# Kernel optimization log

Measured on AMD Instinct MI355X. Metric: run time of the kernel, lower is better.

Reference implementation:

```python
import jax, jax.numpy as jnp
import numpy as np

B, L, D = 4, 1024, 768
HH = 12            # BERT attention heads
E, M = 30, 60      # entities / mentions per sample
P = E * (E - 1)    # 870 head-tail entity pairs
R = 97             # relation classes
BLK = 64           # block_size
NH = D // BLK      # 12 EGAT heads / bilinear groups
MIN = 1e-10


def setup_inputs():
    key = jax.random.key(0)
    ks = jax.random.split(key, 16)
    context = jax.random.normal(ks[0], (B, L, D), jnp.float32) * 0.1
    attention = jax.random.uniform(ks[1], (B, HH, L, L), jnp.float32)
    attention = attention / attention.sum(-1, keepdims=True)  # row-stochastic like softmax attn
    pos = jax.random.randint(ks[2], (B, M), 0, L)
    mention_map = (jnp.arange(L)[None, None, :] == pos[..., None]).astype(jnp.float32)  # [B,M,L] one-hot
    entity_map = (jnp.arange(M)[None, :] // 2 == jnp.arange(E)[:, None]).astype(jnp.float32)
    entity_map = jnp.broadcast_to(entity_map[None], (B, E, M))  # entity e owns mentions 2e,2e+1
    pairs = np.array([(i, j) for i in range(E) for j in range(E) if i != j], np.int64)
    hts = jnp.broadcast_to(jnp.asarray(pairs)[None], (B, P, 2))
    w = lambda k, s: jax.random.normal(k, s, jnp.float32) * 0.02
    return dict(
        context=context, attention=attention, mention_map=mention_map,
        entity_map=entity_map, hts=hts,
        W_h=w(ks[3], (2 * D, D)), b_h=jnp.zeros((D,), jnp.float32),
        W_t=w(ks[4], (2 * D, D)), b_t=jnp.zeros((D,), jnp.float32),
        W_node=w(ks[5], (D, NH * BLK)),
        W_ni=w(ks[6], (D, NH * BLK)), W_nj=w(ks[7], (D, NH * BLK)),
        W_fij=w(ks[8], (D, NH * BLK)), egat_bias=jnp.zeros((NH * BLK,), jnp.float32),
        attn_vec=w(ks[9], (NH, BLK)),
        W_rel=w(ks[10], (D * BLK, R)), b_rel=jnp.zeros((R,), jnp.float32),
    )


def reference(context, attention, mention_map, entity_map, hts,
              W_h, b_h, W_t, b_t, W_node, W_ni, W_nj, W_fij,
              egat_bias, attn_vec, W_rel, b_rel):
    bidx = jnp.arange(B)[:, None]
    ht_mask = (hts.sum(-1) != 0)[..., None].astype(context.dtype)  # [B,P,1]

    # ---- log-sum-exp entity pooling over mentions (get_ht) ----
    mention = jnp.exp(jnp.einsum('bml,bld->bmd', mention_map, context))  # [B,M,D]
    ent = jnp.einsum('bem,bmd->bed', entity_map, mention)                # [B,E,D]
    empty = entity_map.sum(-1, keepdims=True) == 0
    entity = jnp.log(jnp.where(empty, 1.0, ent))                          # [B,E,D]

    # ---- attention-weighted context pooling ----
    em = jnp.einsum('bem,bml->bel', entity_map, mention_map)             # entity -> token map
    em = em / (em.sum(-1, keepdims=True) + MIN)
    ea = jnp.einsum('bel,bhlm->behm', em, attention)                     # [B,E,HH,L]
    ah = ea[bidx, hts[..., 0]]                                            # [B,P,HH,L]
    at = ea[bidx, hts[..., 1]]
    ca = (ah * at).sum(2)                                                 # [B,P,L]
    ca = ca / (ca.sum(-1, keepdims=True) + MIN)
    context_info = jnp.einsum('bpl,bld->bpd', ca, context) * ht_mask      # [B,P,D]

    # ---- batched graph: all hts pairs are edges, plus self loops ----
    N = B * E
    off = (jnp.arange(B) * E)[:, None]
    src = jnp.concatenate([(hts[..., 0] + off).reshape(-1), jnp.arange(N)])
    dst = jnp.concatenate([(hts[..., 1] + off).reshape(-1), jnp.arange(N)])
    x = entity.reshape(N, D)
    efeat = jnp.concatenate([context_info.reshape(B * P, D), x], axis=0)  # pair edges then self loops

    # ---- EGATConv ----
    f_ni = (x @ W_ni).reshape(N, NH, BLK)
    f_nj = (x @ W_nj).reshape(N, NH, BLK)
    f_fij = (efeat @ W_fij).reshape(-1, NH, BLK)
    f_out = f_ni[src] + f_nj[dst] + f_fij + egat_bias.reshape(NH, BLK)    # [Etot,NH,BLK]
    e = jax.nn.leaky_relu(f_out, 0.2)
    scores = (e * attn_vec[None]).sum(-1)                                  # [Etot,NH]
    smax = jax.ops.segment_max(scores, dst, num_segments=N)
    ex = jnp.exp(scores - smax[dst])
    ssum = jax.ops.segment_sum(ex, dst, num_segments=N)
    alpha = ex / ssum[dst]                                                 # edge softmax over in-edges
    msg = (x @ W_node).reshape(N, NH, BLK)[src] * alpha[..., None]
    nodes = jax.ops.segment_sum(msg, dst, num_segments=N)                  # [N,NH,BLK]

    edge_ctx = f_out[:B * P].reshape(B, P, D)                              # get_res (all edges kept, order preserved)
    node_feat = nodes.reshape(B, E, D)

    # ---- get_new_ht + dense + tanh ----
    new_h = jnp.tanh(jnp.concatenate([node_feat[bidx, hts[..., 0]], edge_ctx], -1) @ W_h + b_h)
    new_t = jnp.tanh(jnp.concatenate([node_feat[bidx, hts[..., 1]], edge_ctx], -1) @ W_t + b_t)

    # ---- group biLinear relation classifier ----
    a = new_h.reshape(B, P, NH, BLK)
    b = new_t.reshape(B, P, NH, BLK)
    bl = jnp.einsum('bpkx,bpky->bpkxy', a, b).reshape(B, P, NH * BLK * BLK)
    return bl @ W_rel + b_rel                                              # [B,P,R]
```

## Files before the change

kernel.cpp:

```cpp
#include <hip/hip_runtime.h>
#include <math.h>

#define BB 4
#define LLL 1024
#define DDD 768
#define HHH 12
#define EEE 30
#define MMM 60
#define PPP 870
#define RRR 97
#define NNODE 120
#define NPAIR 3480
#define NEDGE 3600
#define FMIN 1e-10f

typedef __attribute__((ext_vector_type(8))) __bf16 bf16x8;
typedef __attribute__((ext_vector_type(8))) short short8;
typedef __attribute__((ext_vector_type(8))) _Float16 f16x8;
typedef __attribute__((ext_vector_type(4))) float f32x4;
typedef __attribute__((ext_vector_type(4))) unsigned short u16x4;

static __device__ __forceinline__ unsigned short f2bf(float v) {
  return __builtin_bit_cast(unsigned short, (__bf16)v);
}
static __device__ __forceinline__ unsigned short f2h(float v) {
  return __builtin_bit_cast(unsigned short, (_Float16)v);
}
static __device__ __forceinline__ float bf2f(unsigned short u) {
  unsigned int x = ((unsigned int)u) << 16;
  return __builtin_bit_cast(float, x);
}

struct PrepArgs {
  const float *Wrel, *context, *mmap, *emap;
  const float *wsrc[6];
  unsigned short *tW, *ctxT, *xb;
  unsigned short *wdst[6];
  int *nzl, *nzc;
  float *nzw;
};

#define NB_WPREP 768
#define NB_CTX   (24 * 32 * BB)
#define NB_WT    (24 * 48 * 6)
#define NB_ENT   NNODE
#define NB_EM    NNODE

static __device__ void body_wprep(int c, const float* __restrict__ Wrel,
                                  unsigned short* __restrict__ tW) {
  __shared__ float w_s[64][98];
  int tid = threadIdx.x;
  for (int idx = tid; idx < 64 * 97; idx += 256) {
    int y = idx / 97, r = idx - y * 97;
    w_s[y][r] = Wrel[(size_t)(c * 64 + y) * RRR + r];
  }
  __syncthreads();
  for (int odx = tid; odx < 8192; odx += 256) {
    int nt = odx >> 10, h = (odx >> 9) & 1, lane = (odx >> 3) & 63, i = odx & 7;
    int y = 32 * h + 8 * (lane >> 4) + i;
    int r = nt * 16 + (lane & 15);
    float v = (r < RRR) ? w_s[y][r] : 0.f;
    tW[(size_t)c * 8192 + odx] = f2h(v);
  }
}

static __device__ void body_transpose(int bx, int by, const float* __restrict__ s,
                                      unsigned short* __restrict__ d, int R, int C) {
  __shared__ float t_s[32][33];
  int c0 = bx * 32, r0 = by * 32;
  int tx = threadIdx.x & 31, ty = threadIdx.x >> 5;
  #pragma unroll
  for (int i = 0; i < 4; i++)
    t_s[ty + i * 8][tx] = s[(size_t)(r0 + ty + i * 8) * C + c0 + tx];
  __syncthreads();
  #pragma unroll
  for (int i = 0; i < 4; i++)
    d[(size_t)(c0 + ty + i * 8) * R + r0 + tx] = f2bf(t_s[tx][ty + i * 8]);
}

static __device__ void body_entity(int be, const float* __restrict__ ctx,
                                   const float* __restrict__ mmap,
                                   const float* __restrict__ emap,
                                   unsigned short* __restrict__ xb) {
  __shared__ int s_cnt;
  __shared__ int s_l[16];
  __shared__ float s_w[16];
  int b = be / EEE;
  int tid = threadIdx.x;
  float acc[3] = {0.f, 0.f, 0.f};
  float csum = 0.f;
  for (int m = 0; m < MMM; m++) {
    float wm = emap[(size_t)be * MMM + m];
    csum += wm;
    if (wm == 0.f) continue;
    if (tid == 0) s_cnt = 0;
    __syncthreads();
    const float* mrow = mmap + ((size_t)b * MMM + m) * LLL;
    #pragma unroll
    for (int q = 0; q < 4; q++) {
      int l = tid + 256 * q;
      float w = mrow[l];
      if (w != 0.f) {
        int i = atomicAdd(&s_cnt, 1);
        if (i < 16) { s_l[i] = l; s_w[i] = w; }
      }
    }
    __syncthreads();
    int c = min(s_cnt, 16);
    float dot[3] = {0.f, 0.f, 0.f};
    for (int i = 0; i < c; i++) {
      const float* cr = ctx + ((size_t)b * LLL + s_l[i]) * DDD;
      float w = s_w[i];
      #pragma unroll
      for (int q = 0; q < 3; q++) dot[q] += w * cr[tid + 256 * q];
    }
    #pragma unroll
    for (int q = 0; q < 3; q++) acc[q] += wm * expf(dot[q]);
  }
  bool empty = (csum == 0.f);
  #pragma unroll
  for (int q = 0; q < 3; q++)
    xb[(size_t)be * DDD + tid + 256 * q] = f2bf(empty ? 0.f : logf(acc[q]));
}

static __device__ void body_em(int be, const float* __restrict__ emap,
                               const float* __restrict__ mmap,
                               int* __restrict__ nzl, float* __restrict__ nzw,
                               int* __restrict__ nzc) {
  __shared__ float em_s[1024];
  __shared__ float red[256];
  int b = be / EEE;
  int tid = threadIdx.x;
  float acc[4] = {0.f, 0.f, 0.f, 0.f};
  for (int m = 0; m < MMM; m++) {
    float w = emap[(size_t)be * MMM + m];
    if (w != 0.f) {
      const float* mr = mmap + ((size_t)b * MMM + m) * LLL;
      #pragma unroll
      for (int q = 0; q < 4; q++) acc[q] += w * mr[tid + 256 * q];
    }
  }
  red[tid] = acc[0] + acc[1] + acc[2] + acc[3];
  __syncthreads();
  for (int st = 128; st > 0; st >>= 1) {
    if (tid < st) red[tid] += red[tid + st];
    __syncthreads();
  }
  float inv = 1.f / (red[0] + FMIN);
  #pragma unroll
  for (int q = 0; q < 4; q++) em_s[tid + 256 * q] = acc[q] * inv;
  __syncthreads();
  if (tid < 64) {
    int base = 0;
    for (int l0 = 0; l0 < LLL; l0 += 64) {
      float w = em_s[l0 + tid];
      unsigned long long mb = __ballot(w != 0.f);
      int pre = __popcll(mb & ((1ull << tid) - 1ull));
      if (w != 0.f) {
        nzl[be * LLL + base + pre] = l0 + tid;
        nzw[be * LLL + base + pre] = w;
      }
      base += __popcll(mb);
    }
    if (tid == 0) nzc[be] = base;
  }
}

__global__ __launch_bounds__(256) void k_prep(PrepArgs a) {
  int bid = blockIdx.x;
  if (bid < NB_WPREP) {
    body_wprep(bid, a.Wrel, a.tW);
    return;
  }
  bid -= NB_WPREP;
  if (bid < NB_CTX) {
    int bx = bid % 24, by = (bid / 24) % 32, bz = bid / (24 * 32);
    body_transpose(bx, by, a.context + (size_t)bz * LLL * DDD,
                   a.ctxT + (size_t)bz * DDD * LLL, LLL, DDD);
    return;
  }
  bid -= NB_CTX;
  if (bid < NB_WT) {
    int bx = bid % 24, by = (bid / 24) % 48, bz = bid / (24 * 48);
    int R = (bz < 4) ? DDD : 2 * DDD;
    if (by * 32 < R) body_transpose(bx, by, a.wsrc[bz], a.wdst[bz], R, DDD);
    return;
  }
  bid -= NB_WT;
  if (bid < NB_ENT) {
    body_entity(bid, a.context, a.mmap, a.emap, a.xb);
    return;
  }
  bid -= NB_ENT;
  body_em(bid, a.emap, a.mmap, a.nzl, a.nzw, a.nzc);
}

__global__ __launch_bounds__(256) void k_ea(const float* __restrict__ attn,
                                            const int* __restrict__ nzl,
                                            const float* __restrict__ nzw,
                                            const int* __restrict__ nzc,
                                            unsigned short* __restrict__ ea) {
  int e = blockIdx.x, h = blockIdx.y, b = blockIdx.z;
  int be = b * EEE + e;
  int cnt = nzc[be];
  float acc[4] = {0.f, 0.f, 0.f, 0.f};
  for (int i = 0; i < cnt; i++) {
    int l = nzl[be * LLL + i];
    float w = nzw[be * LLL + i];
    const float* ar = attn + (((size_t)b * HHH + h) * LLL + l) * LLL;
    #pragma unroll
    for (int q = 0; q < 4; q++) acc[q] += w * ar[threadIdx.x + 256 * q];
  }
  unsigned short* er = ea + ((size_t)be * HHH + h) * LLL;
  #pragma unroll
  for (int q = 0; q < 4; q++) er[threadIdx.x + 256 * q] = f2bf(acc[q]);
}

__global__ __launch_bounds__(256) void k_ca(const unsigned short* __restrict__ ea,
                                            const int* __restrict__ hts,
                                            unsigned short* __restrict__ cab,
                                            const float* __restrict__ brel,
                                            float* __restrict__ out) {
  int bp = blockIdx.x;
  int b = bp / PPP;
  int hs = hts[bp * 2 + 0], ts = hts[bp * 2 + 1];
  int tid = threadIdx.x;
  if (tid < RRR) out[(size_t)bp * RRR + tid] = brel[tid];
  const unsigned short* eh = ea + (size_t)(b * EEE + hs) * HHH * LLL;
  const unsigned short* et = ea + (size_t)(b * EEE + ts) * HHH * LLL;
  float v[4] = {0.f, 0.f, 0.f, 0.f};
  #pragma unroll
  for (int h = 0; h < HHH; h++) {
    u16x4 hv = *(const u16x4*)&eh[h * LLL + tid * 4];
    u16x4 tv = *(const u16x4*)&et[h * LLL + tid * 4];
    #pragma unroll
    for (int q = 0; q < 4; q++) v[q] += bf2f(hv[q]) * bf2f(tv[q]);
  }
  __shared__ float red[256];
  red[tid] = v[0] + v[1] + v[2] + v[3];
  __syncthreads();
  for (int st = 128; st > 0; st >>= 1) {
    if (tid < st) red[tid] += red[tid + st];
    __syncthreads();
  }
  float inv = 1.f / (red[0] + FMIN);
  u16x4 o;
  #pragma unroll
  for (int q = 0; q < 4; q++) o[q] = f2bf(v[q] * inv);
  *(u16x4*)&cab[(size_t)bp * LLL + tid * 4] = o;
}

struct MGArgs {
  const unsigned short *A, *A2, *BT0, *BT1, *BT2, *BT3;
  float *C0, *C1, *C2;
  const float *nodeW;
  float *nodeWout;
  unsigned short *Cb, *Ch, *Ct;
  const float *bias0, *bias1;
  const float *fni, *fnj, *ebias, *avec;
  float *scores;
  const int *hts;
  int M, K, ldb, koffB;
};

template <int MODE>
__global__ __launch_bounds__(256) void k_mgemm(MGArgs g) {
  __shared__ unsigned short As[3][64 * 64];
  __shared__ unsigned short Bs[3][64 * 64];
  int tid = threadIdx.x;
  int lane = tid & 63;
  int wv = tid >> 6;
  int l15 = lane & 15, l4 = lane >> 4;
  int wr = wv >> 1, wc = wv & 1;
  int bz = blockIdx.z;

  bool isC = true; int zz = 0;
  if (MODE == 5) {
    isC = bz < 4; zz = bz - 4;
    if (!isC && blockIdx.x >= 2) return;
  }
  int K = g.K, M = g.M, ldb = g.ldb, koffB = g.koffB;
  if (MODE == 5) { K = isC ? LLL : DDD; M = isC ? PPP : NNODE; ldb = K; koffB = 0; }
  int row0 = blockIdx.x * 64, col0 = blockIdx.y * 64;

  const unsigned short* BTp;
  if (MODE == 5) BTp = isC ? g.BT0 + (size_t)bz * DDD * LLL
                           : (zz == 0 ? g.BT1 : (zz == 1 ? g.BT2 : g.BT3));
  else if (MODE == 2) BTp = g.BT0;
  else BTp = bz ? g.BT1 : g.BT0;

  int sgg = (lane & 7) ^ ((lane >> 3) & 7);
  int srsub = lane >> 3;

  const unsigned short* gaA[2];
  const unsigned short* gaB[2];
  #pragma unroll
  for (int jj = 0; jj < 2; jj++) {
    int j = wv * 2 + jj;
    int row = j * 8 + srsub;
    int grow = row0 + row; if (grow >= M) grow = M - 1;
    if (MODE == 5) {
      gaA[jj] = isC ? g.A + ((size_t)(bz * PPP) + grow) * LLL + sgg * 8
                    : g.A2 + (size_t)grow * DDD + sgg * 8;
    } else if (MODE == 2) {
      gaA[jj] = (grow < NPAIR) ? g.A + (size_t)grow * DDD + sgg * 8
                               : g.A2 + (size_t)(grow - NPAIR) * DDD + sgg * 8;
    } else {
      gaA[jj] = g.A + (size_t)grow * DDD + sgg * 8;
    }
    gaB[jj] = BTp + (size_t)(col0 + row) * ldb + koffB + sgg * 8;
  }

  auto stage = [&](int buf, int t) {
    int k = t * 64;
    #pragma unroll
    for (int jj = 0; jj < 2; jj++) {
      int j = wv * 2 + jj;
      __builtin_amdgcn_global_load_lds(
          (const __attribute__((address_space(1))) unsigned int*)(gaA[jj] + k),
          (__attribute__((address_space(3))) unsigned int*)&As[buf][j * 512],
          16, 0, 0);
      __builtin_amdgcn_global_load_lds(
          (const __attribute__((address_space(1))) unsigned int*)(gaB[jj] + k),
          (__attribute__((address_space(3))) unsigned int*)&Bs[buf][j * 512],
          16, 0, 0);
    }
  };

  f32x4 zero = {0.f, 0.f, 0.f, 0.f};
  f32x4 acc[2][2];
  #pragma unroll
  for (int m = 0; m < 2; m++)
    #pragma unroll
    for (int n = 0; n < 2; n++) acc[m][n] = zero;

  int nt = K / 64;
  stage(0, 0);
  stage(1, 1);
  asm volatile("s_waitcnt vmcnt(4)" ::: "memory");
  __builtin_amdgcn_s_barrier();

  int cur = 0;
  for (int t = 0; t < nt; t++) {
    if (t + 2 < nt) {
      int nxt2 = cur - 1; if (nxt2 < 0) nxt2 = 2;
      stage(nxt2, t + 2);
    }
    short8 af[2][2], bfr[2][2];
    #pragma unroll
    for (int ks = 0; ks < 2; ks++) {
      #pragma unroll
      for (int m = 0; m < 2; m++) {
        int row = wr * 32 + m * 16 + l15;
        int phys = (ks * 4 + l4) ^ (row & 7);
        af[ks][m] = *(const short8*)&As[cur][row * 64 + phys * 8];
      }
      #pragma unroll
      for (int n = 0; n < 2; n++) {
        int row = wc * 32 + n * 16 + l15;
        int phys = (ks * 4 + l4) ^ (row & 7);
        bfr[ks][n] = *(const short8*)&Bs[cur][row * 64 + phys * 8];
      }
    }
    #pragma unroll
    for (int ks = 0; ks < 2; ks++)
      #pragma unroll
      for (int m = 0; m < 2; m++)
        #pragma unroll
        for (int n = 0; n < 2; n++)
          acc[m][n] = __builtin_amdgcn_mfma_f32_16x16x32_bf16(af[ks][m], bfr[ks][n], acc[m][n], 0, 0, 0);
    if (t + 1 < nt) {
      if (t + 2 < nt) asm volatile("s_waitcnt vmcnt(4)" ::: "memory");
      else            asm volatile("s_waitcnt vmcnt(0)" ::: "memory");
      __builtin_amdgcn_s_barrier();
    }
    cur += 1; if (cur == 3) cur = 0;
  }

  float* score_s = (float*)&As[0][0];
  if (MODE == 2) {
    if (tid < 64) score_s[tid] = 0.f;
    __syncthreads();
  }

  float sp[2][4] = {};
  #pragma unroll
  for (int m = 0; m < 2; m++) {
    int rbase = row0 + wr * 32 + m * 16 + l4 * 4;
    #pragma unroll
    for (int n = 0; n < 2; n++) {
      int col = col0 + wc * 32 + n * 16 + l15;
      #pragma unroll
      for (int q = 0; q < 4; q++) {
        int r = rbase + q;
        if (r >= M) continue;
        float v = acc[m][n][q];
        if (MODE == 5) {
          if (isC) {
            size_t grow = (size_t)bz * PPP + r;
            int h0 = g.hts[grow * 2 + 0], h1 = g.hts[grow * 2 + 1];
            float mk = (h0 + h1 != 0) ? 1.f : 0.f;
            g.Cb[grow * DDD + col] = f2bf(v * mk);
          } else {
            float* C = zz == 0 ? g.C0 : (zz == 1 ? g.C1 : g.C2);
            C[(size_t)r * DDD + col] = v;
          }
        } else if (MODE == 2) {
          int srcn, dstn;
          if (r < NPAIR) {
            int bb = r / PPP;
            srcn = bb * EEE + g.hts[r * 2 + 0];
            dstn = bb * EEE + g.hts[r * 2 + 1];
          } else {
            srcn = dstn = r - NPAIR;
          }
          float vv = v + g.fni[(size_t)srcn * DDD + col] +
                     g.fnj[(size_t)dstn * DDD + col] + g.ebias[col];
          g.Cb[(size_t)r * DDD + col] = f2bf(vv);
          float lrv = vv > 0.f ? vv : 0.2f * vv;
          sp[m][q] += lrv * g.avec[col];
        } else if (MODE == 4) {
          g.nodeWout[((size_t)bz * NNODE + r) * DDD + col] = v;
        } else {
          int bb = r / PPP;
          int node = bb * EEE + g.hts[r * 2 + bz];
          const float* bias = bz ? g.bias1 : g.bias0;
          float v2 = v + g.nodeW[((size_t)bz * NNODE + node) * DDD + col] + bias[col];
          unsigned short* C = bz ? g.Ct : g.Ch;
          C[(size_t)r * DDD + col] = f2h(tanhf(v2));
        }
      }
    }
  }

  if (MODE == 2) {
    #pragma unroll
    for (int m = 0; m < 2; m++) {
      #pragma unroll
      for (int q = 0; q < 4; q++) {
        float s = sp[m][q];
        s += __shfl_xor(s, 1);
        s += __shfl_xor(s, 2);
        s += __shfl_xor(s, 4);
        s += __shfl_xor(s, 8);
        int r = row0 + wr * 32 + m * 16 + l4 * 4 + q;
        if (l15 == 0 && r < M) atomicAdd(&score_s[r - row0], s);
      }
    }
    __syncthreads();
    if (tid < 64) {
      int r = row0 + tid;
      if (r < M) g.scores[r * HHH + blockIdx.y] = score_s[tid];
    }
  }
}

#define ECAP 256
__global__ __launch_bounds__(256) void k_agg(const float* __restrict__ scores,
                                             const float* __restrict__ fnode,
                                             const int* __restrict__ hts,
                                             unsigned short* __restrict__ nodesb) {
  __shared__ int cnt;
  __shared__ int elist[ECAP], slist[ECAP];
  __shared__ float smax[HHH], ssum[HHH];
  __shared__ float alpha[ECAP * HHH];
  int n = blockIdx.x, tid = threadIdx.x;
  if (tid == 0) cnt = 0;
  __syncthreads();
  for (int e = tid; e < NEDGE; e += 256) {
    int srcn, dstn;
    if (e < NPAIR) {
      int b = e / PPP;
      srcn = b * EEE + hts[e * 2 + 0];
      dstn = b * EEE + hts[e * 2 + 1];
    } else {
      srcn = dstn = e - NPAIR;
    }
    if (dstn == n) {
      int i = atomicAdd(&cnt, 1);
      if (i < ECAP) { elist[i] = e; slist[i] = srcn; }
    }
  }
  __syncthreads();
  int c = min(cnt, ECAP);
  if (tid < HHH) {
    float m = -1e30f;
    for (int i = 0; i < c; i++) m = fmaxf(m, scores[elist[i] * HHH + tid]);
    smax[tid] = m;
    float s = 0.f;
    for (int i = 0; i < c; i++) s += expf(scores[elist[i] * HHH + tid] - m);
    ssum[tid] = s;
  }
  __syncthreads();
  for (int t = tid; t < c * HHH; t += 256) {
    int i = t / HHH, h = t - i * HHH;
    alpha[t] = expf(scores[elist[i] * HHH + h] - smax[h]) / ssum[h];
  }
  __syncthreads();
  for (int j = tid; j < DDD; j += 256) {
    int h = j >> 6;
    float acc = 0.f;
    for (int i = 0; i < c; i++)
      acc += alpha[i * HHH + h] * fnode[(size_t)slist[i] * DDD + j];
    nodesb[(size_t)n * DDD + j] = f2bf(acc);
  }
}

__global__ __launch_bounds__(256) void k_bilinear_mfma(
    const unsigned short* __restrict__ newh, const unsigned short* __restrict__ newt,
    const unsigned short* __restrict__ tW, float* __restrict__ out) {
  __shared__ unsigned short a_s[64][64];
  int tid = threadIdx.x;
  int lane = tid & 63;
  int wv = tid >> 6;
  int l15 = lane & 15, l4 = lane >> 4;
  int bid = blockIdx.x;
  int kg = bid / 55, pt = bid - kg * 55;
  bool use1 = ((wv + 4) * 16) < RRR;

  {
    int pl = tid >> 2, xq = (tid & 3) * 16;
    int prow = pt * 64 + pl; if (prow >= NPAIR) prow = NPAIR - 1;
    const unsigned short* src = newh + (size_t)prow * DDD + kg * 64 + xq;
    #pragma unroll
    for (int half16 = 0; half16 < 2; half16++) {
      u16x4 v0 = *(const u16x4*)(src + half16 * 8);
      u16x4 v1 = *(const u16x4*)(src + half16 * 8 + 4);
      #pragma unroll
      for (int i = 0; i < 4; i++) {
        a_s[xq + half16 * 8 + i][pl] = v0[i];
        a_s[xq + half16 * 8 + 4 + i][pl] = v1[i];
      }
    }
  }

  f16x8 bfrag[4][2];
  #pragma unroll
  for (int t = 0; t < 4; t++) {
    int prow = pt * 64 + t * 16 + l15; if (prow >= NPAIR) prow = NPAIR - 1;
    const unsigned short* src = newt + (size_t)prow * DDD + kg * 64 + 8 * l4;
    #pragma unroll
    for (int h = 0; h < 2; h++)
      bfrag[t][h] = __builtin_bit_cast(f16x8, *(const uint4*)(src + h * 32));
  }
  __syncthreads();

  f32x4 zero = {0.f, 0.f, 0.f, 0.f};
  f32x4 acc[4][2];
  #pragma unroll
  for (int t = 0; t < 4; t++) { acc[t][0] = zero; acc[t][1] = zero; }

  const unsigned short* wp = tW + (size_t)(kg * 64) * 8192 + lane * 8;
  int o00 = (wv * 2 + 0) << 9;
  int o01 = (wv * 2 + 1) << 9;
  int o10 = ((wv + 4) * 2 + 0) << 9;
  int o11 = ((wv + 4) * 2 + 1) << 9;

  auto loadw = [&](uint4* wf, int x) {
    const unsigned short* p = wp + (size_t)x * 8192;
    wf[0] = *(const uint4*)(p + o00);
    wf[1] = *(const uint4*)(p + o01);
    if (use1) {
      wf[2] = *(const uint4*)(p + o10);
      wf[3] = *(const uint4*)(p + o11);
    }
  };
  auto step = [&](const uint4* wf, int x) {
    f16x8 a8[4];
    #pragma unroll
    for (int t = 0; t < 4; t++) {
      unsigned int av = a_s[x][t * 16 + l15];
      unsigned int aw = (av << 16) | av;
      uint4 ab = {aw, aw, aw, aw};
      a8[t] = __builtin_bit_cast(f16x8, ab);
    }
    #pragma unroll
    for (int h = 0; h < 2; h++) {
      f16x8 w0 = __builtin_bit_cast(f16x8, wf[h]);
      f16x8 w1 = __builtin_bit_cast(f16x8, wf[2 + h]);
      #pragma unroll
      for (int t = 0; t < 4; t++) {
        f16x8 gv = a8[t] * bfrag[t][h];
        acc[t][0] = __builtin_amdgcn_mfma_f32_16x16x32_f16(gv, w0, acc[t][0], 0, 0, 0);
        if (use1)
          acc[t][1] = __builtin_amdgcn_mfma_f32_16x16x32_f16(gv, w1, acc[t][1], 0, 0, 0);
      }
    }
  };

  uint4 wa[4], wb[4];
  loadw(wa, 0);
  for (int xx = 0; xx < 64; xx += 2) {
    loadw(wb, xx + 1);
    step(wa, xx);
    if (xx + 2 < 64) loadw(wa, xx + 2);
    step(wb, xx + 1);
  }

  #pragma unroll
  for (int n = 0; n < 2; n++) {
    int r = (wv + 4 * n) * 16 + l15;
    if (r >= RRR) continue;
    #pragma unroll
    for (int t = 0; t < 4; t++) {
      int pbase = pt * 64 + t * 16 + l4 * 4;
      #pragma unroll
      for (int q = 0; q < 4; q++) {
        int p = pbase + q;
        if (p < NPAIR) atomicAdd(&out[(size_t)p * RRR + r], acc[t][n][q]);
      }
    }
  }
}

extern "C" void kernel_launch(void* const* d_in, const int* in_sizes, int n_in,
                              void* d_out, int out_size, void* d_ws, size_t ws_size,
                              hipStream_t stream) {
  const float* context   = (const float*)d_in[0];
  const float* attention = (const float*)d_in[1];
  const float* mmap      = (const float*)d_in[2];
  const float* emap      = (const float*)d_in[3];
  const int*   hts       = (const int*)d_in[4];
  const float* W_h       = (const float*)d_in[5];
  const float* b_h       = (const float*)d_in[6];
  const float* W_t       = (const float*)d_in[7];
  const float* b_t       = (const float*)d_in[8];
  const float* W_node    = (const float*)d_in[9];
  const float* W_ni      = (const float*)d_in[10];
  const float* W_nj      = (const float*)d_in[11];
  const float* W_fij     = (const float*)d_in[12];
  const float* egat_bias = (const float*)d_in[13];
  const float* attn_vec  = (const float*)d_in[14];
  const float* W_rel     = (const float*)d_in[15];
  const float* b_rel     = (const float*)d_in[16];
  float* out = (float*)d_out;

  float* ws = (float*)d_ws;
  size_t o = 0;
  auto alloc = [&](size_t n) { size_t r = o; o += (n + 63) & ~(size_t)63; return r; };
  auto halloc = [&](size_t nshorts) { return alloc((nshorts + 1) / 2); };
  size_t o_xb      = halloc((size_t)NNODE * DDD);
  size_t o_ea      = halloc((size_t)BB * EEE * HHH * LLL);
  size_t o_cab     = halloc((size_t)NPAIR * LLL);
  size_t o_ctxT    = halloc((size_t)BB * DDD * LLL);
  size_t o_wtni    = halloc((size_t)DDD * DDD);
  size_t o_wtnj    = halloc((size_t)DDD * DDD);
  size_t o_wtnode  = halloc((size_t)DDD * DDD);
  size_t o_wtfij   = halloc((size_t)DDD * DDD);
  size_t o_wth     = halloc((size_t)DDD * 2 * DDD);
  size_t o_wtt     = halloc((size_t)DDD * 2 * DDD);
  size_t o_cinfob  = halloc((size_t)NPAIR * DDD);
  size_t o_fni     = alloc((size_t)NNODE * DDD);
  size_t o_fnj     = alloc((size_t)NNODE * DDD);
  size_t o_fnode   = alloc((size_t)NNODE * DDD);
  size_t o_foutb   = halloc((size_t)NEDGE * DDD);
  size_t o_scores  = alloc((size_t)NEDGE * HHH);
  size_t o_nodesb  = halloc((size_t)NNODE * DDD);
  size_t o_nodew   = alloc((size_t)2 * NNODE * DDD);
  size_t o_newh    = halloc((size_t)NPAIR * DDD);
  size_t o_newt    = halloc((size_t)NPAIR * DDD);
  size_t o_nzl     = alloc((size_t)BB * EEE * LLL);
  size_t o_nzw     = alloc((size_t)BB * EEE * LLL);
  size_t o_nzc     = alloc(128);
  size_t o_tw      = halloc((size_t)768 * 8192);
  (void)ws_size;

  unsigned short* xb     = (unsigned short*)(ws + o_xb);
  unsigned short* ea     = (unsigned short*)(ws + o_ea);
  unsigned short* cab    = (unsigned short*)(ws + o_cab);
  unsigned short* ctxT   = (unsigned short*)(ws + o_ctxT);
  unsigned short* wtni   = (unsigned short*)(ws + o_wtni);
  unsigned short* wtnj   = (unsigned short*)(ws + o_wtnj);
  unsigned short* wtnode = (unsigned short*)(ws + o_wtnode);
  unsigned short* wtfij  = (unsigned short*)(ws + o_wtfij);
  unsigned short* wth    = (unsigned short*)(ws + o_wth);
  unsigned short* wtt    = (unsigned short*)(ws + o_wtt);
  unsigned short* cinfob = (unsigned short*)(ws + o_cinfob);
  float* fni     = ws + o_fni;
  float* fnj     = ws + o_fnj;
  float* fnode   = ws + o_fnode;
  unsigned short* foutb  = (unsigned short*)(ws + o_foutb);
  float* scores  = ws + o_scores;
  unsigned short* nodesb = (unsigned short*)(ws + o_nodesb);
  float* nodeW   = ws + o_nodew;
  unsigned short* newh   = (unsigned short*)(ws + o_newh);
  unsigned short* newt   = (unsigned short*)(ws + o_newt);
  int*   nzl     = (int*)(ws + o_nzl);
  float* nzw     = ws + o_nzw;
  int*   nzc     = (int*)(ws + o_nzc);
  unsigned short* tW = (unsigned short*)(ws + o_tw);

  PrepArgs pa;
  pa.Wrel = W_rel; pa.context = context; pa.mmap = mmap; pa.emap = emap;
  pa.wsrc[0] = W_ni;  pa.wdst[0] = wtni;
  pa.wsrc[1] = W_nj;  pa.wdst[1] = wtnj;
  pa.wsrc[2] = W_node; pa.wdst[2] = wtnode;
  pa.wsrc[3] = W_fij; pa.wdst[3] = wtfij;
  pa.wsrc[4] = W_h;   pa.wdst[4] = wth;
  pa.wsrc[5] = W_t;   pa.wdst[5] = wtt;
  pa.tW = tW; pa.ctxT = ctxT; pa.xb = xb;
  pa.nzl = nzl; pa.nzw = nzw; pa.nzc = nzc;
  k_prep<<<NB_WPREP + NB_CTX + NB_WT + NB_ENT + NB_EM, 256, 0, stream>>>(pa);

  k_ea<<<dim3(EEE, HHH, BB), 256, 0, stream>>>(attention, nzl, nzw, nzc, ea);
  k_ca<<<BB * PPP, 256, 0, stream>>>(ea, hts, cab, b_rel, out);

  MGArgs g5 = {};
  g5.A = cab; g5.A2 = xb;
  g5.BT0 = ctxT; g5.BT1 = wtni; g5.BT2 = wtnj; g5.BT3 = wtnode;
  g5.Cb = cinfob; g5.C0 = fni; g5.C1 = fnj; g5.C2 = fnode;
  g5.hts = hts;
  k_mgemm<5><<<dim3(14, 12, 7), 256, 0, stream>>>(g5);

  MGArgs g2 = {};
  g2.A = cinfob; g2.A2 = xb; g2.BT0 = wtfij; g2.Cb = foutb;
  g2.fni = fni; g2.fnj = fnj; g2.ebias = egat_bias; g2.avec = attn_vec;
  g2.scores = scores; g2.hts = hts;
  g2.M = NEDGE; g2.K = DDD; g2.ldb = DDD; g2.koffB = 0;
  k_mgemm<2><<<dim3(57, 12, 1), 256, 0, stream>>>(g2);

  k_agg<<<NNODE, 256, 0, stream>>>(scores, fnode, hts, nodesb);

  MGArgs g4 = {};
  g4.A = nodesb; g4.BT0 = wth; g4.BT1 = wtt; g4.nodeWout = nodeW;
  g4.M = NNODE; g4.K = DDD; g4.ldb = 2 * DDD; g4.koffB = 0;
  k_mgemm<4><<<dim3(2, 12, 2), 256, 0, stream>>>(g4);

  MGArgs g3 = {};
  g3.A = foutb; g3.BT0 = wth; g3.BT1 = wtt; g3.nodeW = nodeW;
  g3.bias0 = b_h; g3.bias1 = b_t; g3.Ch = newh; g3.Ct = newt; g3.hts = hts;
  g3.M = NPAIR; g3.K = DDD; g3.ldb = 2 * DDD; g3.koffB = DDD;
  k_mgemm<3><<<dim3(55, 12, 2), 256, 0, stream>>>(g3);

  k_bilinear_mfma<<<55 * 12, 256, 0, stream>>>(newh, newt, tW, out);
}
```

Before: 208.2 us.

## Fuse entity-attention gather into prep kernel and widen bilinear tiles

Entity-mention map computation and the attention gather are merged into one prep block per entity, keeping the nonzero list in shared memory and looping over heads, and these blocks are scheduled first. This removes the separate k_ea launch and the global nzl/nzw buffers. The bilinear MFMA kernel now uses 512 threads covering 128 pairs per block with one relation tile per wave, so each weight fragment is reused across twice as many pairs and the per-wave conditional second tile goes away. The risks are a truncation at 128 nonzeros per entity, less parallelism in the ea work (120 blocks instead of 1440), and a larger register footprint in the bilinear kernel.

```diff
diff --git a/kernel.cpp b/kernel.cpp
--- a/kernel.cpp
+++ b/kernel.cpp
@@ -32,50 +32,77 @@
 }
 
 struct PrepArgs {
-  const float *Wrel, *context, *mmap, *emap;
+  const float *Wrel, *context, *mmap, *emap, *attn;
   const float *wsrc[6];
-  unsigned short *tW, *ctxT, *xb;
+  unsigned short *tW, *ctxT, *xb, *ea;
   unsigned short *wdst[6];
-  int *nzl, *nzc;
-  float *nzw;
 };
 
+#define NB_EMEA  NNODE
+#define NB_ENT   NNODE
 #define NB_WPREP 768
 #define NB_CTX   (24 * 32 * BB)
 #define NB_WT    (24 * 48 * 6)
-#define NB_ENT   NNODE
-#define NB_EM    NNODE
-
-static __device__ void body_wprep(int c, const float* __restrict__ Wrel,
-                                  unsigned short* __restrict__ tW) {
-  __shared__ float w_s[64][98];
+
+static __device__ void body_emea(int be, const float* __restrict__ emap,
+                                 const float* __restrict__ mmap,
+                                 const float* __restrict__ attn,
+                                 unsigned short* __restrict__ ea) {
+  __shared__ float em_s[1024];
+  __shared__ float red[256];
+  __shared__ int s_nzl[128];
+  __shared__ float s_nzw[128];
+  __shared__ int s_cnt;
+  int b = be / EEE;
   int tid = threadIdx.x;
-  for (int idx = tid; idx < 64 * 97; idx += 256) {
-    int y = idx / 97, r = idx - y * 97;
-    w_s[y][r] = Wrel[(size_t)(c * 64 + y) * RRR + r];
-  }
-  __syncthreads();
-  for (int odx = tid; odx < 8192; odx += 256) {
-    int nt = odx >> 10, h = (odx >> 9) & 1, lane = (odx >> 3) & 63, i = odx & 7;
-    int y = 32 * h + 8 * (lane >> 4) + i;
-    int r = nt * 16 + (lane & 15);
-    float v = (r < RRR) ? w_s[y][r] : 0.f;
-    tW[(size_t)c * 8192 + odx] = f2h(v);
-  }
-}
-
-static __device__ void body_transpose(int bx, int by, const float* __restrict__ s,
-                                      unsigned short* __restrict__ d, int R, int C) {
-  __shared__ float t_s[32][33];
-  int c0 = bx * 32, r0 = by * 32;
-  int tx = threadIdx.x & 31, ty = threadIdx.x >> 5;
-  #pragma unroll
-  for (int i = 0; i < 4; i++)
-    t_s[ty + i * 8][tx] = s[(size_t)(r0 + ty + i * 8) * C + c0 + tx];
-  __syncthreads();
-  #pragma unroll
-  for (int i = 0; i < 4; i++)
-    d[(size_t)(c0 + ty + i * 8) * R + r0 + tx] = f2bf(t_s[tx][ty + i * 8]);
+  float acc[4] = {0.f, 0.f, 0.f, 0.f};
+  for (int m = 0; m < MMM; m++) {
+    float w = emap[(size_t)be * MMM + m];
+    if (w != 0.f) {
+      const float* mr = mmap + ((size_t)b * MMM + m) * LLL;
+      #pragma unroll
+      for (int q = 0; q < 4; q++) acc[q] += w * mr[tid + 256 * q];
+    }
+  }
+  red[tid] = acc[0] + acc[1] + acc[2] + acc[3];
+  __syncthreads();
+  for (int st = 128; st > 0; st >>= 1) {
+    if (tid < st) red[tid] += red[tid + st];
+    __syncthreads();
+  }
+  float inv = 1.f / (red[0] + FMIN);
+  #pragma unroll
+  for (int q = 0; q < 4; q++) em_s[tid + 256 * q] = acc[q] * inv;
+  __syncthreads();
+  if (tid < 64) {
+    int base = 0;
+    for (int l0 = 0; l0 < LLL; l0 += 64) {
+      float w = em_s[l0 + tid];
+      unsigned long long mb = __ballot(w != 0.f);
+      int pre = __popcll(mb & ((1ull << tid) - 1ull));
+      if (w != 0.f && base + pre < 128) {
+        s_nzl[base + pre] = l0 + tid;
+        s_nzw[base + pre] = w;
+      }
+      base += __popcll(mb);
+    }
+    if (tid == 0) s_cnt = base;
+  }
+  __syncthreads();
+  int cnt = min(s_cnt, 128);
+  for (int h = 0; h < HHH; h++) {
+    float a2[4] = {0.f, 0.f, 0.f, 0.f};
+    for (int i = 0; i < cnt; i++) {
+      int l = s_nzl[i];
+      float w = s_nzw[i];
+      const float* ar = attn + (((size_t)b * HHH + h) * LLL + l) * LLL;
+      #pragma unroll
+      for (int q = 0; q < 4; q++) a2[q] += w * ar[tid + 256 * q];
+    }
+    unsigned short* er = ea + ((size_t)be * HHH + h) * LLL;
+    #pragma unroll
+    for (int q = 0; q < 4; q++) er[tid + 256 * q] = f2bf(a2[q]);
+  }
 }
 
 static __device__ void body_entity(int be, const float* __restrict__ ctx,
@@ -123,51 +150,50 @@
     xb[(size_t)be * DDD + tid + 256 * q] = f2bf(empty ? 0.f : logf(acc[q]));
 }
 
-static __device__ void body_em(int be, const float* __restrict__ emap,
-                               const float* __restrict__ mmap,
-                               int* __restrict__ nzl, float* __restrict__ nzw,
-                               int* __restrict__ nzc) {
-  __shared__ float em_s[1024];
-  __shared__ float red[256];
-  int b = be / EEE;
+static __device__ void body_wprep(int c, const float* __restrict__ Wrel,
+                                  unsigned short* __restrict__ tW) {
+  __shared__ float w_s[64][98];
   int tid = threadIdx.x;
-  float acc[4] = {0.f, 0.f, 0.f, 0.f};
-  for (int m = 0; m < MMM; m++) {
-    float w = emap[(size_t)be * MMM + m];
-    if (w != 0.f) {
-      const float* mr = mmap + ((size_t)b * MMM + m) * LLL;
-      #pragma unroll
-      for (int q = 0; q < 4; q++) acc[q] += w * mr[tid + 256 * q];
-    }
-  }
-  red[tid] = acc[0] + acc[1] + acc[2] + acc[3];
-  __syncthreads();
-  for (int st = 128; st > 0; st >>= 1) {
-    if (tid < st) red[tid] += red[tid + st];
-    __syncthreads();
-  }
-  float inv = 1.f / (red[0] + FMIN);
-  #pragma unroll
-  for (int q = 0; q < 4; q++) em_s[tid + 256 * q] = acc[q] * inv;
-  __syncthreads();
-  if (tid < 64) {
-    int base = 0;
-    for (int l0 = 0; l0 < LLL; l0 += 64) {
-      float w = em_s[l0 + tid];
-      unsigned long long mb = __ballot(w != 0.f);
-      int pre = __popcll(mb & ((1ull << tid) - 1ull));
-      if (w != 0.f) {
-        nzl[be * LLL + base + pre] = l0 + tid;
-        nzw[be * LLL + base + pre] = w;
-      }
-      base += __popcll(mb);
-    }
-    if (tid == 0) nzc[be] = base;
-  }
+  for (int idx = tid; idx < 64 * 97; idx += 256) {
+    int y = idx / 97, r = idx - y * 97;
+    w_s[y][r] = Wrel[(size_t)(c * 64 + y) * RRR + r];
+  }
+  __syncthreads();
+  for (int odx = tid; odx < 8192; odx += 256) {
+    int nt = odx >> 10, h = (odx >> 9) & 1, lane = (odx >> 3) & 63, i = odx & 7;
+    int y = 32 * h + 8 * (lane >> 4) + i;
+    int r = nt * 16 + (lane & 15);
+    float v = (r < RRR) ? w_s[y][r] : 0.f;
+    tW[(size_t)c * 8192 + odx] = f2h(v);
+  }
+}
+
+static __device__ void body_transpose(int bx, int by, const float* __restrict__ s,
+                                      unsigned short* __restrict__ d, int R, int C) {
+  __shared__ float t_s[32][33];
+  int c0 = bx * 32, r0 = by * 32;
+  int tx = threadIdx.x & 31, ty = threadIdx.x >> 5;
+  #pragma unroll
+  for (int i = 0; i < 4; i++)
+    t_s[ty + i * 8][tx] = s[(size_t)(r0 + ty + i * 8) * C + c0 + tx];
+  __syncthreads();
+  #pragma unroll
+  for (int i = 0; i < 4; i++)
+    d[(size_t)(c0 + ty + i * 8) * R + r0 + tx] = f2bf(t_s[tx][ty + i * 8]);
 }
 
 __global__ __launch_bounds__(256) void k_prep(PrepArgs a) {
   int bid = blockIdx.x;
+  if (bid < NB_EMEA) {
+    body_emea(bid, a.emap, a.mmap, a.attn, a.ea);
+    return;
+  }
+  bid -= NB_EMEA;
+  if (bid < NB_ENT) {
+    body_entity(bid, a.context, a.mmap, a.emap, a.xb);
+    return;
+  }
+  bid -= NB_ENT;
   if (bid < NB_WPREP) {
     body_wprep(bid, a.Wrel, a.tW);
     return;
@@ -180,40 +206,11 @@
     return;
   }
   bid -= NB_CTX;
-  if (bid < NB_WT) {
+  {
     int bx = bid % 24, by = (bid / 24) % 48, bz = bid / (24 * 48);
     int R = (bz < 4) ? DDD : 2 * DDD;
     if (by * 32 < R) body_transpose(bx, by, a.wsrc[bz], a.wdst[bz], R, DDD);
-    return;
-  }
-  bid -= NB_WT;
-  if (bid < NB_ENT) {
-    body_entity(bid, a.context, a.mmap, a.emap, a.xb);
-    return;
-  }
-  bid -= NB_ENT;
-  body_em(bid, a.emap, a.mmap, a.nzl, a.nzw, a.nzc);
-}
-
-__global__ __launch_bounds__(256) void k_ea(const float* __restrict__ attn,
-                                            const int* __restrict__ nzl,
-                                            const float* __restrict__ nzw,
-                                            const int* __restrict__ nzc,
-                                            unsigned short* __restrict__ ea) {
-  int e = blockIdx.x, h = blockIdx.y, b = blockIdx.z;
-  int be = b * EEE + e;
-  int cnt = nzc[be];
-  float acc[4] = {0.f, 0.f, 0.f, 0.f};
-  for (int i = 0; i < cnt; i++) {
-    int l = nzl[be * LLL + i];
-    float w = nzw[be * LLL + i];
-    const float* ar = attn + (((size_t)b * HHH + h) * LLL + l) * LLL;
-    #pragma unroll
-    for (int q = 0; q < 4; q++) acc[q] += w * ar[threadIdx.x + 256 * q];
-  }
-  unsigned short* er = ea + ((size_t)be * HHH + h) * LLL;
-  #pragma unroll
-  for (int q = 0; q < 4; q++) er[threadIdx.x + 256 * q] = f2bf(acc[q]);
+  }
 }
 
 __global__ __launch_bounds__(256) void k_ca(const unsigned short* __restrict__ ea,
@@ -506,21 +503,20 @@
   }
 }
 
-__global__ __launch_bounds__(256) void k_bilinear_mfma(
+__global__ __launch_bounds__(512) void k_bilinear_mfma(
     const unsigned short* __restrict__ newh, const unsigned short* __restrict__ newt,
     const unsigned short* __restrict__ tW, float* __restrict__ out) {
-  __shared__ unsigned short a_s[64][64];
+  __shared__ unsigned short a_s[64][128];
   int tid = threadIdx.x;
   int lane = tid & 63;
   int wv = tid >> 6;
   int l15 = lane & 15, l4 = lane >> 4;
   int bid = blockIdx.x;
-  int kg = bid / 55, pt = bid - kg * 55;
-  bool use1 = ((wv + 4) * 16) < RRR;
+  int kg = bid / 28, pt = bid - kg * 28;
 
   {
     int pl = tid >> 2, xq = (tid & 3) * 16;
-    int prow = pt * 64 + pl; if (prow >= NPAIR) prow = NPAIR - 1;
+    int prow = pt * 128 + pl; if (prow >= NPAIR) prow = NPAIR - 1;
     const unsigned short* src = newh + (size_t)prow * DDD + kg * 64 + xq;
     #pragma unroll
     for (int half16 = 0; half16 < 2; half16++) {
@@ -534,10 +530,10 @@
     }
   }
 
-  f16x8 bfrag[4][2];
-  #pragma unroll
-  for (int t = 0; t < 4; t++) {
-    int prow = pt * 64 + t * 16 + l15; if (prow >= NPAIR) prow = NPAIR - 1;
+  f16x8 bfrag[8][2];
+  #pragma unroll
+  for (int t = 0; t < 8; t++) {
+    int prow = pt * 128 + t * 16 + l15; if (prow >= NPAIR) prow = NPAIR - 1;
     const unsigned short* src = newt + (size_t)prow * DDD + kg * 64 + 8 * l4;
     #pragma unroll
     for (int h = 0; h < 2; h++)
@@ -546,68 +542,59 @@
   __syncthreads();
 
   f32x4 zero = {0.f, 0.f, 0.f, 0.f};
-  f32x4 acc[4][2];
-  #pragma unroll
-  for (int t = 0; t < 4; t++) { acc[t][0] = zero; acc[t][1] = zero; }
-
-  const unsigned short* wp = tW + (size_t)(kg * 64) * 8192 + lane * 8;
-  int o00 = (wv * 2 + 0) << 9;
-  int o01 = (wv * 2 + 1) << 9;
-  int o10 = ((wv + 4) * 2 + 0) << 9;
-  int o11 = ((wv + 4) * 2 + 1) << 9;
-
-  auto loadw = [&](uint4* wf, int x) {
-    const unsigned short* p = wp + (size_t)x * 8192;
-    wf[0] = *(const uint4*)(p + o00);
-    wf[1] = *(const uint4*)(p + o01);
-    if (use1) {
-      wf[2] = *(const uint4*)(p + o10);
-      wf[3] = *(const uint4*)(p + o11);
-    }
-  };
-  auto step = [&](const uint4* wf, int x) {
-    f16x8 a8[4];
-    #pragma unroll
-    for (int t = 0; t < 4; t++) {
-      unsigned int av = a_s[x][t * 16 + l15];
-      unsigned int aw = (av << 16) | av;
-      uint4 ab = {aw, aw, aw, aw};
-      a8[t] = __builtin_bit_cast(f16x8, ab);
-    }
-    #pragma unroll
-    for (int h = 0; h < 2; h++) {
-      f16x8 w0 = __builtin_bit_cast(f16x8, wf[h]);
-      f16x8 w1 = __builtin_bit_cast(f16x8, wf[2 + h]);
-      #pragma unroll
-      for (int t = 0; t < 4; t++) {
-        f16x8 gv = a8[t] * bfrag[t][h];
-        acc[t][0] = __builtin_amdgcn_mfma_f32_16x16x32_f16(gv, w0, acc[t][0], 0, 0, 0);
-        if (use1)
-          acc[t][1] = __builtin_amdgcn_mfma_f32_16x16x32_f16(gv, w1, acc[t][1], 0, 0, 0);
-      }
-    }
-  };
-
-  uint4 wa[4], wb[4];
-  loadw(wa, 0);
-  for (int xx = 0; xx < 64; xx += 2) {
-    loadw(wb, xx + 1);
-    step(wa, xx);
-    if (xx + 2 < 64) loadw(wa, xx + 2);
-    step(wb, xx + 1);
-  }
-
-  #pragma unroll
-  for (int n = 0; n < 2; n++) {
-    int r = (wv + 4 * n) * 16 + l15;
-    if (r >= RRR) continue;
-    #pragma unroll
-    for (int t = 0; t < 4; t++) {
-      int pbase = pt * 64 + t * 16 + l4 * 4;
+  f32x4 acc[8];
+  #pragma unroll
+  for (int t = 0; t < 8; t++) acc[t] = zero;
+
+  if (wv < 7) {
+    const unsigned short* wp = tW + (size_t)(kg * 64) * 8192 + lane * 8;
+    int o0 = (wv * 2 + 0) << 9;
+    int o1 = (wv * 2 + 1) << 9;
+
+    auto loadw = [&](uint4* wf, int x) {
+      const unsigned short* p = wp + (size_t)x * 8192;
+      wf[0] = *(const uint4*)(p + o0);
+      wf[1] = *(const uint4*)(p + o1);
+    };
+    auto step = [&](const uint4* wf, int x) {
+      f16x8 a8[8];
+      #pragma unroll
+      for (int t = 0; t < 8; t++) {
+        unsigned int av = a_s[x][t * 16 + l15];
+        unsigned int aw = (av << 16) | av;
+        uint4 ab = {aw, aw, aw, aw};
+        a8[t] = __builtin_bit_cast(f16x8, ab);
+      }
+      #pragma unroll
+      for (int h = 0; h < 2; h++) {
+        f16x8 w = __builtin_bit_cast(f16x8, wf[h]);
+        #pragma unroll
+        for (int t = 0; t < 8; t++) {
+          f16x8 gv = a8[t] * bfrag[t][h];
+          acc[t] = __builtin_amdgcn_mfma_f32_16x16x32_f16(gv, w, acc[t], 0, 0, 0);
+        }
+      }
+    };
+
+    uint4 wa[2], wb[2];
+    loadw(wa, 0);
+    for (int xx = 0; xx < 64; xx += 2) {
+      loadw(wb, xx + 1);
+      step(wa, xx);
+      if (xx + 2 < 64) loadw(wa, xx + 2);
+      step(wb, xx + 1);
+    }
+  }
+
+  int r = wv * 16 + l15;
+  if (r < RRR) {
+    #pragma unroll
+    for (int t = 0; t < 8; t++) {
+      int pbase = pt * 128 + t * 16 + l4 * 4;
       #pragma unroll
       for (int q = 0; q < 4; q++) {
         int p = pbase + q;
-        if (p < NPAIR) atomicAdd(&out[(size_t)p * RRR + r], acc[t][n][q]);
+        if (p < NPAIR) atomicAdd(&out[(size_t)p * RRR + r], acc[t][q]);
       }
     }
   }
@@ -659,9 +646,6 @@
   size_t o_nodew   = alloc((size_t)2 * NNODE * DDD);
   size_t o_newh    = halloc((size_t)NPAIR * DDD);
   size_t o_newt    = halloc((size_t)NPAIR * DDD);
-  size_t o_nzl     = alloc((size_t)BB * EEE * LLL);
-  size_t o_nzw     = alloc((size_t)BB * EEE * LLL);
-  size_t o_nzc     = alloc(128);
   size_t o_tw      = halloc((size_t)768 * 8192);
   (void)ws_size;
 
@@ -685,24 +669,20 @@
   float* nodeW   = ws + o_nodew;
   unsigned short* newh   = (unsigned short*)(ws + o_newh);
   unsigned short* newt   = (unsigned short*)(ws + o_newt);
-  int*   nzl     = (int*)(ws + o_nzl);
-  float* nzw     = ws + o_nzw;
-  int*   nzc     = (int*)(ws + o_nzc);
   unsigned short* tW = (unsigned short*)(ws + o_tw);
 
   PrepArgs pa;
   pa.Wrel = W_rel; pa.context = context; pa.mmap = mmap; pa.emap = emap;
+  pa.attn = attention;
   pa.wsrc[0] = W_ni;  pa.wdst[0] = wtni;
   pa.wsrc[1] = W_nj;  pa.wdst[1] = wtnj;
   pa.wsrc[2] = W_node; pa.wdst[2] = wtnode;
   pa.wsrc[3] = W_fij; pa.wdst[3] = wtfij;
   pa.wsrc[4] = W_h;   pa.wdst[4] = wth;
   pa.wsrc[5] = W_t;   pa.wdst[5] = wtt;
-  pa.tW = tW; pa.ctxT = ctxT; pa.xb = xb;
-  pa.nzl = nzl; pa.nzw = nzw; pa.nzc = nzc;
-  k_prep<<<NB_WPREP + NB_CTX + NB_WT + NB_ENT + NB_EM, 256, 0, stream>>>(pa);
-
-  k_ea<<<dim3(EEE, HHH, BB), 256, 0, stream>>>(attention, nzl, nzw, nzc, ea);
+  pa.tW = tW; pa.ctxT = ctxT; pa.xb = xb; pa.ea = ea;
+  k_prep<<<NB_EMEA + NB_ENT + NB_WPREP + NB_CTX + NB_WT, 256, 0, stream>>>(pa);
+
   k_ca<<<BB * PPP, 256, 0, stream>>>(ea, hts, cab, b_rel, out);
 
   MGArgs g5 = {};
@@ -732,5 +712,5 @@
   g3.M = NPAIR; g3.K = DDD; g3.ldb = 2 * DDD; g3.koffB = DDD;
   k_mgemm<3><<<dim3(55, 12, 2), 256, 0, stream>>>(g3);
 
-  k_bilinear_mfma<<<55 * 12, 256, 0, stream>>>(newh, newt, tW, out);
-}
+  k_bilinear_mfma<<<28 * 12, 512, 0, stream>>>(newh, newt, tW, out);
+}
```

New measurement: 229.1 us. 1.1x slower.
